# Performance work log

Measured on AMD Instinct MI355X. Metric: run time of the kernel, lower is better.

The kernel has to match this reference:

```python
import jax, jax.numpy as jnp
import numpy as np

N_ATOM_FEATS = 64
N_RBF = 10
N_CONV = 3
N_HIDDEN = 64
N_NODES = 50000
N_EDGES = 800000
N_GRAPHS = 512


def setup_inputs() -> dict:
    key = jax.random.key(0)
    ks = jax.random.split(key, 32)
    d = {}
    d["x_ids"] = jax.random.randint(ks[0], (N_NODES,), 0, 95)
    d["edge_index"] = jax.random.randint(ks[1], (2, N_EDGES), 0, N_NODES)
    d["edge_attr"] = jax.random.uniform(ks[2], (N_EDGES,), jnp.float32) * 6.0  # distances in [0,6)
    d["batch"] = jnp.sort(jax.random.randint(ks[3], (N_NODES,), 0, N_GRAPHS))
    # parameters
    def lin(k, fan_in, shape):
        return jax.random.normal(k, shape, jnp.float32) / np.sqrt(fan_in)
    d["emb"] = jax.random.normal(ks[4], (95, N_ATOM_FEATS), jnp.float32)
    d["blk_W1"] = lin(ks[5], N_ATOM_FEATS, (N_CONV, N_ATOM_FEATS, N_ATOM_FEATS))
    d["blk_b1"] = jnp.zeros((N_CONV, N_ATOM_FEATS), jnp.float32)
    d["blk_We"] = lin(ks[6], N_RBF, (N_CONV, N_RBF, N_ATOM_FEATS))
    d["blk_be"] = jnp.zeros((N_CONV, N_ATOM_FEATS), jnp.float32)
    d["blk_W2"] = lin(ks[7], N_ATOM_FEATS, (N_CONV, N_ATOM_FEATS, N_ATOM_FEATS))
    d["blk_b2"] = jnp.zeros((N_CONV, N_ATOM_FEATS), jnp.float32)
    d["Ws"] = lin(ks[8], N_ATOM_FEATS, (N_ATOM_FEATS, 2 * N_HIDDEN))
    d["bs"] = jnp.zeros((2 * N_HIDDEN,), jnp.float32)
    d["Wbg1"] = lin(ks[9], 2 * N_HIDDEN, (2 * N_HIDDEN, N_HIDDEN))
    d["bbg1"] = jnp.zeros((N_HIDDEN,), jnp.float32)
    d["Wbg2"] = lin(ks[10], N_HIDDEN, (N_HIDDEN, 1))
    d["bbg2"] = jnp.zeros((1,), jnp.float32)
    d["Weh1"] = lin(ks[11], 2 * N_HIDDEN, (2 * N_HIDDEN, N_HIDDEN))
    d["beh1"] = jnp.zeros((N_HIDDEN,), jnp.float32)
    d["Weh2"] = lin(ks[12], N_HIDDEN, (N_HIDDEN, 1))
    d["beh2"] = jnp.zeros((1,), jnp.float32)
    return d


def reference(x_ids, edge_index, edge_attr, batch, emb,
              blk_W1, blk_b1, blk_We, blk_be, blk_W2, blk_b2,
              Ws, bs, Wbg1, bbg1, Wbg2, bbg2, Weh1, beh1, Weh2, beh2):
    src, dst = edge_index[0], edge_index[1]
    # embedding lookup [N, F]
    x = emb[x_ids]
    # Gaussian smearing RBF: [E, n_rbf]
    offset = jnp.linspace(0.0, 6.0, N_RBF).astype(edge_attr.dtype)
    coeff = -0.5 / (offset[1] - offset[0]) ** 2
    e = jnp.exp(coeff * (edge_attr[:, None] - offset) ** 2)
    # interaction blocks (SchNet-style CFConv with residual)
    for i in range(N_CONV):
        h = x @ blk_W1[i] + blk_b1[i]                     # [N, F]
        f = e @ blk_We[i] + blk_be[i]                     # [E, F] edge filters
        m = h[src] * f                                    # [E, F] messages
        agg = jax.ops.segment_sum(m, dst, num_segments=N_NODES)
        x = x + agg @ blk_W2[i] + blk_b2[i]
        x = jax.nn.softplus(x)
    # global mean pool over graphs
    sums = jax.ops.segment_sum(x, batch, num_segments=N_GRAPHS)
    cnts = jax.ops.segment_sum(jnp.ones((x.shape[0],), x.dtype), batch, num_segments=N_GRAPHS)
    c = sums / jnp.maximum(cnts, 1.0)[:, None]
    c = jax.nn.relu(c @ Ws + bs)                          # [G, 2H]
    out_bg = jax.nn.relu(c @ Wbg1 + bbg1) @ Wbg2 + bbg2   # [G, 1]
    out_eh = jax.nn.relu(c @ Weh1 + beh1) @ Weh2 + beh2   # [G, 1]
    return (out_bg, out_eh)
```

## Files before the change

kernel.cpp:

```cpp
#include <hip/hip_runtime.h>
#include <hip/hip_fp16.h>
#include <cstddef>


#define BSH 8

#define RBF_C0 1.0f
#define RBF_C1 0.60653065971f
#define RBF_C2 0.13533528324f
#define RBF_C3 0.011108996538f
#define RBF_C4 3.3546262790e-4f
#define RBF_C5 3.7266531720e-6f
#define RBF_C6 1.5229979745e-8f
#define RBF_C7 2.2897348457e-11f
#define RBF_C8 1.2664165549e-14f
#define RBF_C9 2.5767043600e-18f

__device__ __forceinline__ float softplusf(float v) {
    return fmaxf(v, 0.0f) + log1pf(__expf(-fabsf(v)));
}

__device__ __forceinline__ float row_gemv(const float4* __restrict__ xr,
                                          const float w[64], float bj) {
    float a0 = bj, a1 = 0.f, a2 = 0.f, a3 = 0.f;
#pragma unroll
    for (int q = 0; q < 4; ++q) {
        float4 v0 = xr[4 * q + 0], v1 = xr[4 * q + 1];
        float4 v2 = xr[4 * q + 2], v3 = xr[4 * q + 3];
        a0 = fmaf(v0.x, w[16 * q + 0], a0);  a0 = fmaf(v0.y, w[16 * q + 1], a0);
        a0 = fmaf(v0.z, w[16 * q + 2], a0);  a0 = fmaf(v0.w, w[16 * q + 3], a0);
        a1 = fmaf(v1.x, w[16 * q + 4], a1);  a1 = fmaf(v1.y, w[16 * q + 5], a1);
        a1 = fmaf(v1.z, w[16 * q + 6], a1);  a1 = fmaf(v1.w, w[16 * q + 7], a1);
        a2 = fmaf(v2.x, w[16 * q + 8], a2);  a2 = fmaf(v2.y, w[16 * q + 9], a2);
        a2 = fmaf(v2.z, w[16 * q + 10], a2); a2 = fmaf(v2.w, w[16 * q + 11], a2);
        a3 = fmaf(v3.x, w[16 * q + 12], a3); a3 = fmaf(v3.y, w[16 * q + 13], a3);
        a3 = fmaf(v3.z, w[16 * q + 14], a3); a3 = fmaf(v3.w, w[16 * q + 15], a3);
    }
    return (a0 + a1) + (a2 + a3);
}

__device__ __forceinline__ float filt_ab(const float wp[10], float bj, float A, float B) {
    float P = wp[9];
    P = fmaf(B, P, wp[8]); P = fmaf(B, P, wp[7]); P = fmaf(B, P, wp[6]);
    P = fmaf(B, P, wp[5]); P = fmaf(B, P, wp[4]); P = fmaf(B, P, wp[3]);
    P = fmaf(B, P, wp[2]); P = fmaf(B, P, wp[1]); P = fmaf(B, P, wp[0]);
    return fmaf(A, P, bj);
}

__global__ void k_pre(const int* __restrict__ dst, int* __restrict__ deg,
                      const int* __restrict__ batch, int* __restrict__ gstart,
                      const int* __restrict__ ids, const float* __restrict__ emb,
                      const float* __restrict__ W1, const float* __restrict__ b1,
                      float* __restrict__ x, __half* __restrict__ hA,
                      int n_edges, int n_nodes, int n_graphs) {
    int tid = blockIdx.x * blockDim.x + threadIdx.x;
    int nth = gridDim.x * blockDim.x;
    for (int e = tid; e < n_edges; e += nth) atomicAdd(&deg[dst[e]], 1);
    for (int n = tid; n < n_nodes; n += nth) {
        int b = batch[n];
        int prev = (n == 0) ? -1 : batch[n - 1];
        for (int g = prev + 1; g <= b; ++g) gstart[g] = n;
        if (n == n_nodes - 1)
            for (int g = b + 1; g <= n_graphs; ++g) gstart[g] = n_nodes;
    }
    int lane = threadIdx.x & 63;
    int gw = __builtin_amdgcn_readfirstlane(tid >> 6);
    int nw = nth >> 6;
    float w[64];
#pragma unroll
    for (int k = 0; k < 64; ++k) w[k] = W1[k * 64 + lane];
    float bj = b1[lane];
    for (int n = gw; n < n_nodes; n += nw) {
        int id = __builtin_amdgcn_readfirstlane(ids[n]);
        const float4* xr = (const float4*)(emb + id * 64);
        float v = row_gemv(xr, w, bj);
        x[n * 64 + lane] = emb[id * 64 + lane];
        hA[n * 64 + lane] = __float2half(v);
    }
}

__global__ void k_scana(const int* __restrict__ deg, int* __restrict__ off_,
                        int* __restrict__ bsum, int n) {
    __shared__ int s[256];
    int i = blockIdx.x * 256 + threadIdx.x;
    int v = (i < n) ? deg[i] : 0;
    s[threadIdx.x] = v;
    __syncthreads();
    for (int off = 1; off < 256; off <<= 1) {
        int t = (threadIdx.x >= off) ? s[threadIdx.x - off] : 0;
        __syncthreads();
        s[threadIdx.x] += t;
        __syncthreads();
    }
    if (i < n) off_[i + 1] = s[threadIdx.x];
    if (threadIdx.x == 255) bsum[blockIdx.x] = s[255];
}

__global__ void k_scanb(int* __restrict__ bsum, int nb) {
    __shared__ int s[256];
    int v = ((int)threadIdx.x < nb) ? bsum[threadIdx.x] : 0;
    s[threadIdx.x] = v;
    __syncthreads();
    for (int off = 1; off < 256; off <<= 1) {
        int t = (threadIdx.x >= off) ? s[threadIdx.x - off] : 0;
        __syncthreads();
        s[threadIdx.x] += t;
        __syncthreads();
    }
    if ((int)threadIdx.x < nb) bsum[threadIdx.x] = s[threadIdx.x] - v;
}

__global__ void k_scanc(const int* __restrict__ deg, const int* __restrict__ bsum,
                        int* __restrict__ off_, int* __restrict__ cursor,
                        int* __restrict__ bcursor, int n) {
    int i = blockIdx.x * blockDim.x + threadIdx.x;
    if (i < n) {
        int incl = off_[i + 1] + bsum[i >> 8];
        off_[i + 1] = incl;
        cursor[i] = incl - deg[i];
        if (((i + 1) & ((1 << BSH) - 1)) == 0)
            bcursor[(i + 1) >> BSH] = incl;
    }
    if (i == 0) { off_[0] = 0; bcursor[0] = 0; }
}

__global__ __launch_bounds__(256) void k_scat1(
        const int* __restrict__ src, const int* __restrict__ dst,
        const float* __restrict__ dist, int* __restrict__ bcursor,
        int4* __restrict__ tmp, int n_edges) {
    __shared__ int hist[256], sofs[256], hbase[256], lcur[256];
    __shared__ int4 buf[1024];
    const int t = threadIdx.x;
    const int base = blockIdx.x << 10;

    hist[t] = 0;
    __syncthreads();

    int bk[4]; int4 pl[4];
#pragma unroll
    for (int i = 0; i < 4; ++i) {
        int e = base + (i << 8) + t;
        if (e < n_edges) {
            int d_ = dst[e];
            float dd = dist[e];
            float A = __expf(-1.125f * dd * dd);
            float B = __expf(1.5f * dd);
            pl[i] = make_int4(src[e] << 6, __float_as_int(A), __float_as_int(B), d_);
            bk[i] = d_ >> BSH;
            atomicAdd(&hist[bk[i]], 1);
        } else bk[i] = -1;
    }
    __syncthreads();

    int mycnt = hist[t];
    for (int off = 1; off < 256; off <<= 1) {
        int v = (t >= off) ? hist[t - off] : 0;
        __syncthreads();
        hist[t] += v;
        __syncthreads();
    }
    sofs[t] = hist[t] - mycnt;
    lcur[t] = hist[t] - mycnt;
    if (mycnt > 0) hbase[t] = atomicAdd(&bcursor[t], mycnt);
    __syncthreads();

#pragma unroll
    for (int i = 0; i < 4; ++i) {
        if (bk[i] >= 0) {
            int ls = atomicAdd(&lcur[bk[i]], 1);
            buf[ls] = pl[i];
        }
    }
    __syncthreads();

    int tot = n_edges - base; if (tot > 1024) tot = 1024;
    for (int s = t; s < tot; s += 256) {
        int4 p = buf[s];
        int b = p.w >> BSH;
        tmp[hbase[b] + (s - sofs[b])] = p;
    }
}

__global__ __launch_bounds__(256) void k_scat2(
        const int4* __restrict__ tmp, const int* __restrict__ off_,
        int* __restrict__ cursor, int4* __restrict__ psort, int n_nodes) {
    int b = blockIdx.x;
    int s0 = off_[b << BSH];
    int hi = (b + 1) << BSH; if (hi > n_nodes) hi = n_nodes;
    int s1 = off_[hi];
    int s = s0 + threadIdx.x;
    for (; s + 768 < s1; s += 1024) {
        int4 p0 = tmp[s], p1 = tmp[s + 256], p2 = tmp[s + 512], p3 = tmp[s + 768];
        int q0 = atomicAdd(&cursor[p0.w], 1);
        int q1 = atomicAdd(&cursor[p1.w], 1);
        int q2 = atomicAdd(&cursor[p2.w], 1);
        int q3 = atomicAdd(&cursor[p3.w], 1);
        psort[q0] = p0; psort[q1] = p1; psort[q2] = p2; psort[q3] = p3;
    }
    for (; s < s1; s += 256) {
        int4 p = tmp[s];
        psort[atomicAdd(&cursor[p.w], 1)] = p;
    }
}

__global__ void k_scatter(const int* __restrict__ src, const int* __restrict__ dst,
                          const float* __restrict__ dist, int* __restrict__ cursor,
                          int4* __restrict__ psort, int n_edges) {
    int e = blockIdx.x * blockDim.x + threadIdx.x;
    if (e >= n_edges) return;
    int t = dst[e];
    int pos = atomicAdd(&cursor[t], 1);
    float d = dist[e];
    float A = __expf(-1.125f * d * d);
    float B = __expf(1.5f * d);
    psort[pos] = make_int4(src[e] << 6, __float_as_int(A), __float_as_int(B), 0);
}

__global__ __launch_bounds__(256, 8) void k_gather(
        const int4* __restrict__ ps, const int* __restrict__ off,
        const __half* __restrict__ h,
        const float* __restrict__ We, const float* __restrict__ be,
        float* __restrict__ agg, int n_nodes) {
    int lane = threadIdx.x & 63;
    int gw = __builtin_amdgcn_readfirstlane((blockIdx.x * blockDim.x + threadIdx.x) >> 6);
    int nw = (gridDim.x * blockDim.x) >> 6;

    const float C[10] = {RBF_C0, RBF_C1, RBF_C2, RBF_C3, RBF_C4,
                         RBF_C5, RBF_C6, RBF_C7, RBF_C8, RBF_C9};
    float wp[10];
#pragma unroll
    for (int r = 0; r < 10; ++r) wp[r] = We[r * 64 + lane] * C[r];
    float bj = be[lane];

    for (int n = gw; n < n_nodes; n += nw) {
        int k0 = off[n], k1 = off[n + 1];
        float acc = 0.0f;
        int k = k0;
        for (; k + 8 <= k1; k += 8) {
            int4 p0 = ps[k + 0], p1 = ps[k + 1], p2 = ps[k + 2], p3 = ps[k + 3];
            int4 p4 = ps[k + 4], p5 = ps[k + 5], p6 = ps[k + 6], p7 = ps[k + 7];
            float g0 = __half2float(h[p0.x + lane]);
            float g1 = __half2float(h[p1.x + lane]);
            float g2 = __half2float(h[p2.x + lane]);
            float g3 = __half2float(h[p3.x + lane]);
            float g4 = __half2float(h[p4.x + lane]);
            float g5 = __half2float(h[p5.x + lane]);
            float g6 = __half2float(h[p6.x + lane]);
            float g7 = __half2float(h[p7.x + lane]);
            acc = fmaf(g0, filt_ab(wp, bj, __int_as_float(p0.y), __int_as_float(p0.z)), acc);
            acc = fmaf(g1, filt_ab(wp, bj, __int_as_float(p1.y), __int_as_float(p1.z)), acc);
            acc = fmaf(g2, filt_ab(wp, bj, __int_as_float(p2.y), __int_as_float(p2.z)), acc);
            acc = fmaf(g3, filt_ab(wp, bj, __int_as_float(p3.y), __int_as_float(p3.z)), acc);
            acc = fmaf(g4, filt_ab(wp, bj, __int_as_float(p4.y), __int_as_float(p4.z)), acc);
            acc = fmaf(g5, filt_ab(wp, bj, __int_as_float(p5.y), __int_as_float(p5.z)), acc);
            acc = fmaf(g6, filt_ab(wp, bj, __int_as_float(p6.y), __int_as_float(p6.z)), acc);
            acc = fmaf(g7, filt_ab(wp, bj, __int_as_float(p7.y), __int_as_float(p7.z)), acc);
        }
        for (; k + 4 <= k1; k += 4) {
            int4 p0 = ps[k + 0], p1 = ps[k + 1], p2 = ps[k + 2], p3 = ps[k + 3];
            float g0 = __half2float(h[p0.x + lane]);
            float g1 = __half2float(h[p1.x + lane]);
            float g2 = __half2float(h[p2.x + lane]);
            float g3 = __half2float(h[p3.x + lane]);
            acc = fmaf(g0, filt_ab(wp, bj, __int_as_float(p0.y), __int_as_float(p0.z)), acc);
            acc = fmaf(g1, filt_ab(wp, bj, __int_as_float(p1.y), __int_as_float(p1.z)), acc);
            acc = fmaf(g2, filt_ab(wp, bj, __int_as_float(p2.y), __int_as_float(p2.z)), acc);
            acc = fmaf(g3, filt_ab(wp, bj, __int_as_float(p3.y), __int_as_float(p3.z)), acc);
        }
        for (; k < k1; ++k) {
            int4 p = ps[k];
            float g = __half2float(h[p.x + lane]);
            acc = fmaf(g, filt_ab(wp, bj, __int_as_float(p.y), __int_as_float(p.z)), acc);
        }
        agg[n * 64 + lane] = acc;
    }
}

__global__ __launch_bounds__(512) void k_epi(
        const float* __restrict__ agg, float* __restrict__ x,
        const float* __restrict__ W2, const float* __restrict__ b2,
        const float* __restrict__ W1n, const float* __restrict__ b1n,
        __half* __restrict__ hout, int n_nodes, int do_next) {
    __shared__ float B1[64 * 65];
    const int t = threadIdx.x;
    const int lane = t & 63;
    const int wid = __builtin_amdgcn_readfirstlane(t >> 6);
    const int base = blockIdx.x << 6;
    const int nv = min(64, n_nodes - base);

#pragma unroll
    for (int i = 0; i < 2; ++i) {
        int f = ((wid * 2 + i) << 8) + (lane << 2);
        int r = f >> 6, c = f & 63;
        int rs = min(r, nv - 1);
        const float4 v = *(const float4*)(agg + (((size_t)(base + rs)) << 6) + c);
        B1[r * 65 + c + 0] = v.x; B1[r * 65 + c + 1] = v.y;
        B1[r * 65 + c + 2] = v.z; B1[r * 65 + c + 3] = v.w;
    }
    __syncthreads();

    float o[8];
#pragma unroll
    for (int jj = 0; jj < 8; ++jj) o[jj] = 0.0f;
#pragma unroll 4
    for (int k = 0; k < 64; ++k) {
        float a = B1[lane * 65 + k];
        const float4* w4 = (const float4*)(W2 + (k << 6) + (wid << 3));
        float4 wa = w4[0], wb = w4[1];
        o[0] = fmaf(a, wa.x, o[0]); o[1] = fmaf(a, wa.y, o[1]);
        o[2] = fmaf(a, wa.z, o[2]); o[3] = fmaf(a, wa.w, o[3]);
        o[4] = fmaf(a, wb.x, o[4]); o[5] = fmaf(a, wb.y, o[5]);
        o[6] = fmaf(a, wb.z, o[6]); o[7] = fmaf(a, wb.w, o[7]);
    }
    __syncthreads();

#pragma unroll
    for (int i = 0; i < 2; ++i) {
        int f = ((wid * 2 + i) << 8) + (lane << 2);
        int r = f >> 6, c = f & 63;
        int rs = min(r, nv - 1);
        const float4 v = *(const float4*)(x + (((size_t)(base + rs)) << 6) + c);
        B1[r * 65 + c + 0] = v.x; B1[r * 65 + c + 1] = v.y;
        B1[r * 65 + c + 2] = v.z; B1[r * 65 + c + 3] = v.w;
    }
    __syncthreads();

#pragma unroll
    for (int jj = 0; jj < 8; ++jj) {
        int j = (wid << 3) + jj;
        float xv = B1[lane * 65 + j];
        float xn = softplusf(xv + o[jj] + b2[j]);
        B1[lane * 65 + j] = xn;
    }
    __syncthreads();

#pragma unroll
    for (int rr = 0; rr < 8; ++rr) {
        int r = (wid << 3) + rr;
        if (r < nv) x[(((size_t)(base + r)) << 6) + lane] = B1[r * 65 + lane];
    }

    if (do_next) {
        float o2[8];
#pragma unroll
        for (int jj = 0; jj < 8; ++jj) o2[jj] = b1n[(wid << 3) + jj];
#pragma unroll 4
        for (int k = 0; k < 64; ++k) {
            float xk = B1[lane * 65 + k];
            const float4* w4 = (const float4*)(W1n + (k << 6) + (wid << 3));
            float4 wa = w4[0], wb = w4[1];
            o2[0] = fmaf(xk, wa.x, o2[0]); o2[1] = fmaf(xk, wa.y, o2[1]);
            o2[2] = fmaf(xk, wa.z, o2[2]); o2[3] = fmaf(xk, wa.w, o2[3]);
            o2[4] = fmaf(xk, wb.x, o2[4]); o2[5] = fmaf(xk, wb.y, o2[5]);
            o2[6] = fmaf(xk, wb.z, o2[6]); o2[7] = fmaf(xk, wb.w, o2[7]);
        }
        __syncthreads();
#pragma unroll
        for (int jj = 0; jj < 8; ++jj)
            B1[lane * 65 + (wid << 3) + jj] = o2[jj];
        __syncthreads();
#pragma unroll
        for (int rr = 0; rr < 8; ++rr) {
            int r = (wid << 3) + rr;
            if (r < nv)
                hout[(((size_t)(base + r)) << 6) + lane] = __float2half(B1[r * 65 + lane]);
        }
    }
}

__global__ __launch_bounds__(256, 6) void k_conv(
        const int4* __restrict__ ps, const int* __restrict__ off,
        const __half* __restrict__ h,
        const float* __restrict__ We, const float* __restrict__ be,
        const float* __restrict__ W2, const float* __restrict__ b2,
        const float* __restrict__ W1n, const float* __restrict__ b1n,
        float* __restrict__ x, __half* __restrict__ hout,
        int n_nodes, int do_next) {
    int lane = threadIdx.x & 63;
    int gw = __builtin_amdgcn_readfirstlane((blockIdx.x * blockDim.x + threadIdx.x) >> 6);
    int nw = (gridDim.x * blockDim.x) >> 6;

    const float C[10] = {RBF_C0, RBF_C1, RBF_C2, RBF_C3, RBF_C4,
                         RBF_C5, RBF_C6, RBF_C7, RBF_C8, RBF_C9};
    float wp[10];
#pragma unroll
    for (int r = 0; r < 10; ++r) wp[r] = We[r * 64 + lane] * C[r];
    float bj  = be[lane];
    float b2j = b2[lane];
    float b1j = do_next ? b1n[lane] : 0.0f;

    for (int n = gw; n < n_nodes; n += nw) {
        int k0 = off[n], k1 = off[n + 1];
        float acc = 0.0f;
        int k = k0;
        for (; k + 8 <= k1; k += 8) {
            int4 p0 = ps[k + 0], p1 = ps[k + 1], p2 = ps[k + 2], p3 = ps[k + 3];
            int4 p4 = ps[k + 4], p5 = ps[k + 5], p6 = ps[k + 6], p7 = ps[k + 7];
            float g0 = __half2float(h[p0.x + lane]);
            float g1 = __half2float(h[p1.x + lane]);
            float g2 = __half2float(h[p2.x + lane]);
            float g3 = __half2float(h[p3.x + lane]);
            float g4 = __half2float(h[p4.x + lane]);
            float g5 = __half2float(h[p5.x + lane]);
            float g6 = __half2float(h[p6.x + lane]);
            float g7 = __half2float(h[p7.x + lane]);
            acc = fmaf(g0, filt_ab(wp, bj, __int_as_float(p0.y), __int_as_float(p0.z)), acc);
            acc = fmaf(g1, filt_ab(wp, bj, __int_as_float(p1.y), __int_as_float(p1.z)), acc);
            acc = fmaf(g2, filt_ab(wp, bj, __int_as_float(p2.y), __int_as_float(p2.z)), acc);
            acc = fmaf(g3, filt_ab(wp, bj, __int_as_float(p3.y), __int_as_float(p3.z)), acc);
            acc = fmaf(g4, filt_ab(wp, bj, __int_as_float(p4.y), __int_as_float(p4.z)), acc);
            acc = fmaf(g5, filt_ab(wp, bj, __int_as_float(p5.y), __int_as_float(p5.z)), acc);
            acc = fmaf(g6, filt_ab(wp, bj, __int_as_float(p6.y), __int_as_float(p6.z)), acc);
            acc = fmaf(g7, filt_ab(wp, bj, __int_as_float(p7.y), __int_as_float(p7.z)), acc);
        }
        for (; k + 4 <= k1; k += 4) {
            int4 p0 = ps[k + 0], p1 = ps[k + 1], p2 = ps[k + 2], p3 = ps[k + 3];
            float g0 = __half2float(h[p0.x + lane]);
            float g1 = __half2float(h[p1.x + lane]);
            float g2 = __half2float(h[p2.x + lane]);
            float g3 = __half2float(h[p3.x + lane]);
            acc = fmaf(g0, filt_ab(wp, bj, __int_as_float(p0.y), __int_as_float(p0.z)), acc);
            acc = fmaf(g1, filt_ab(wp, bj, __int_as_float(p1.y), __int_as_float(p1.z)), acc);
            acc = fmaf(g2, filt_ab(wp, bj, __int_as_float(p2.y), __int_as_float(p2.z)), acc);
            acc = fmaf(g3, filt_ab(wp, bj, __int_as_float(p3.y), __int_as_float(p3.z)), acc);
        }
        for (; k < k1; ++k) {
            int4 p = ps[k];
            float g = __half2float(h[p.x + lane]);
            acc = fmaf(g, filt_ab(wp, bj, __int_as_float(p.y), __int_as_float(p.z)), acc);
        }
        float o0 = b2j + x[n * 64 + lane];
        float o1 = 0.f, o2 = 0.f, o3 = 0.f;
#pragma unroll 4
        for (int kk = 0; kk < 16; ++kk) {
            o0 = fmaf(__shfl(acc, kk),      W2[(kk)      * 64 + lane], o0);
            o1 = fmaf(__shfl(acc, kk + 16), W2[(kk + 16) * 64 + lane], o1);
            o2 = fmaf(__shfl(acc, kk + 32), W2[(kk + 32) * 64 + lane], o2);
            o3 = fmaf(__shfl(acc, kk + 48), W2[(kk + 48) * 64 + lane], o3);
        }
        float xn = softplusf((o0 + o1) + (o2 + o3));
        x[n * 64 + lane] = xn;
        if (do_next) {
            float q0 = b1j, q1 = 0.f, q2 = 0.f, q3 = 0.f;
#pragma unroll 4
            for (int kk = 0; kk < 16; ++kk) {
                q0 = fmaf(__shfl(xn, kk),      W1n[(kk)      * 64 + lane], q0);
                q1 = fmaf(__shfl(xn, kk + 16), W1n[(kk + 16) * 64 + lane], q1);
                q2 = fmaf(__shfl(xn, kk + 32), W1n[(kk + 32) * 64 + lane], q2);
                q3 = fmaf(__shfl(xn, kk + 48), W1n[(kk + 48) * 64 + lane], q3);
            }
            hout[n * 64 + lane] = __float2half((q0 + q1) + (q2 + q3));
        }
    }
}

__global__ void k_poolhead(const float* __restrict__ x, const int* __restrict__ gstart,
                           const float* __restrict__ Ws, const float* __restrict__ bs,
                           const float* __restrict__ Wbg1, const float* __restrict__ bbg1,
                           const float* __restrict__ Wbg2, const float* __restrict__ bbg2,
                           const float* __restrict__ Weh1, const float* __restrict__ beh1,
                           const float* __restrict__ Weh2, const float* __restrict__ beh2,
                           float* __restrict__ out, int n_graphs) {
    __shared__ float red[256];
    __shared__ float c[64];
    __shared__ float h1[128];
    int g = blockIdx.x;
    int t = threadIdx.x, j = t & 63, part = t >> 6;
    int s0 = gstart[g], s1 = gstart[g + 1];
    float acc = 0.0f;
    for (int n = s0 + part; n < s1; n += 4) acc += x[n * 64 + j];
    red[t] = acc;
    __syncthreads();
    if (part == 0)
        c[j] = (red[j] + red[64 + j] + red[128 + j] + red[192 + j]) /
               fmaxf((float)(s1 - s0), 1.0f);
    __syncthreads();
    if (t < 128) {
        float av = bs[t];
#pragma unroll 8
        for (int k = 0; k < 64; ++k) av = fmaf(c[k], Ws[k * 128 + t], av);
        h1[t] = fmaxf(av, 0.0f);
    }
    __syncthreads();
    if (t < 128) {
        const float* W1p = (t < 64) ? Wbg1 : Weh1;
        const float* b1p = (t < 64) ? bbg1 : beh1;
        const float* W2p = (t < 64) ? Wbg2 : Weh2;
        float b2v = (t < 64) ? bbg2[0] : beh2[0];
        int ln = t & 63;
        float a2 = b1p[ln];
#pragma unroll 8
        for (int k = 0; k < 128; ++k) a2 = fmaf(h1[k], W1p[k * 64 + ln], a2);
        a2 = fmaxf(a2, 0.0f);
        float pr = a2 * W2p[ln];
#pragma unroll
        for (int off = 32; off > 0; off >>= 1) pr += __shfl_down(pr, off);
        if (ln == 0) out[(t < 64 ? 0 : n_graphs) + g] = pr + b2v;
    }
}

extern "C" void kernel_launch(void* const* d_in, const int* in_sizes, int n_in,
                              void* d_out, int out_size, void* d_ws, size_t ws_size,
                              hipStream_t stream) {
    const int*   x_ids = (const int*)d_in[0];
    const int*   eidx  = (const int*)d_in[1];
    const float* eattr = (const float*)d_in[2];
    const int*   batch = (const int*)d_in[3];
    const float* emb   = (const float*)d_in[4];
    const float* W1    = (const float*)d_in[5];
    const float* b1    = (const float*)d_in[6];
    const float* We    = (const float*)d_in[7];
    const float* be    = (const float*)d_in[8];
    const float* W2    = (const float*)d_in[9];
    const float* b2    = (const float*)d_in[10];
    const float* Ws_   = (const float*)d_in[11];
    const float* bs_   = (const float*)d_in[12];
    const float* Wbg1  = (const float*)d_in[13];
    const float* bbg1  = (const float*)d_in[14];
    const float* Wbg2  = (const float*)d_in[15];
    const float* bbg2  = (const float*)d_in[16];
    const float* Weh1  = (const float*)d_in[17];
    const float* beh1  = (const float*)d_in[18];
    const float* Weh2  = (const float*)d_in[19];
    const float* beh2  = (const float*)d_in[20];

    int n_nodes  = in_sizes[0];
    int n_edges  = in_sizes[2];
    int n_graphs = out_size / 2;
    const int* src = eidx;
    const int* dst = eidx + n_edges;
    int nbuck = (n_nodes + (1 << BSH) - 1) >> BSH;
    int nbc = (nbuck < 256 ? 256 : nbuck) + 4;

    size_t base_bytes =
        (size_t)n_nodes * 64 * sizeof(float)
      + (size_t)n_nodes * 64 * sizeof(__half) * 2
      + (size_t)n_edges * sizeof(int4)
      + (size_t)n_nodes * sizeof(int) * 2
      + (size_t)(n_nodes + 1) * sizeof(int)
      + 256 * sizeof(int)
      + (size_t)(n_graphs + 1) * sizeof(int)
      + (size_t)nbc * sizeof(int);
    size_t agg_bytes = (size_t)n_nodes * 64 * sizeof(float);
    size_t tmp_bytes = (size_t)n_edges * sizeof(int4);
    size_t aggtmp_bytes = agg_bytes > tmp_bytes ? agg_bytes : tmp_bytes;
    int use_split = (ws_size >= base_bytes + aggtmp_bytes + 1024) ? 1 : 0;

    char* p = (char*)d_ws;
    float* x     = (float*)p;   p += (size_t)n_nodes * 64 * sizeof(float);
    __half* hA   = (__half*)p;  p += (size_t)n_nodes * 64 * sizeof(__half);
    __half* hB   = (__half*)p;  p += (size_t)n_nodes * 64 * sizeof(__half);
    int4* psort  = (int4*)p;    p += (size_t)n_edges * sizeof(int4);
    int* deg     = (int*)p;     p += (size_t)n_nodes * sizeof(int);
    int* off_    = (int*)p;     p += (size_t)(n_nodes + 1) * sizeof(int);
    int* cursor  = (int*)p;     p += (size_t)n_nodes * sizeof(int);
    int* bsum    = (int*)p;     p += 256 * sizeof(int);
    int* gstart  = (int*)p;     p += (size_t)(n_graphs + 1) * sizeof(int);
    int* bcursor = (int*)p;     p += (size_t)nbc * sizeof(int);
    float* agg   = (float*)p;
    int4* tmp    = (int4*)p;
    float* out   = (float*)d_out;

    int nchunks = (n_nodes + 255) / 256;
    int nbE = (n_edges + 255) / 256;
    int nbN = (n_nodes + 255) / 256;
    int ntile = (n_nodes + 63) / 64;
    int nbS1 = (n_edges + 1023) / 1024;

    hipMemsetAsync(deg, 0, (size_t)n_nodes * sizeof(int), stream);
    k_pre<<<nbE, 256, 0, stream>>>(dst, deg, batch, gstart, x_ids, emb, W1, b1,
                                   x, hA, n_edges, n_nodes, n_graphs);
    k_scana<<<nchunks, 256, 0, stream>>>(deg, off_, bsum, n_nodes);
    k_scanb<<<1, 256, 0, stream>>>(bsum, nchunks);
    k_scanc<<<nbN, 256, 0, stream>>>(deg, bsum, off_, cursor, bcursor, n_nodes);

    if (use_split) {
        k_scat1<<<nbS1, 256, 0, stream>>>(src, dst, eattr, bcursor, tmp, n_edges);
        k_scat2<<<nbuck, 256, 0, stream>>>(tmp, off_, cursor, psort, n_nodes);
        k_gather<<<4096, 256, 0, stream>>>(psort, off_, hA, We, be, agg, n_nodes);
        k_epi<<<ntile, 512, 0, stream>>>(agg, x, W2, b2,
                                         W1 + 4096, b1 + 64, hB, n_nodes, 1);
        k_gather<<<4096, 256, 0, stream>>>(psort, off_, hB, We + 640, be + 64, agg, n_nodes);
        k_epi<<<ntile, 512, 0, stream>>>(agg, x, W2 + 4096, b2 + 64,
                                         W1 + 8192, b1 + 128, hA, n_nodes, 1);
        k_gather<<<4096, 256, 0, stream>>>(psort, off_, hA, We + 1280, be + 128, agg, n_nodes);
        k_epi<<<ntile, 512, 0, stream>>>(agg, x, W2 + 8192, b2 + 128,
                                         nullptr, nullptr, nullptr, n_nodes, 0);
    } else {
        k_scatter<<<nbE, 256, 0, stream>>>(src, dst, eattr, cursor, psort, n_edges);
        k_conv<<<4096, 256, 0, stream>>>(psort, off_, hA, We, be, W2, b2,
                                         W1 + 4096, b1 + 64, x, hB, n_nodes, 1);
        k_conv<<<4096, 256, 0, stream>>>(psort, off_, hB, We + 640, be + 64,
                                         W2 + 4096, b2 + 64,
                                         W1 + 8192, b1 + 128, x, hA, n_nodes, 1);
        k_conv<<<4096, 256, 0, stream>>>(psort, off_, hA, We + 1280, be + 128,
                                         W2 + 8192, b2 + 128,
                                         nullptr, nullptr, x, nullptr, n_nodes, 0);
    }

    k_poolhead<<<n_graphs, 256, 0, stream>>>(x, gstart, Ws_, bs_, Wbg1, bbg1, Wbg2, bbg2,
                                             Weh1, beh1, Weh2, beh2, out, n_graphs);
}
```

Before: 380.9 us.

## Split gather into two feature-half passes with two edges per wavefront

The per-node gather kernel now handles only 32 of the 64 features per launch. Each half-wave processes alternate edges, and the two partial sums are combined with a cross-lane shuffle. Each layer launches the kernel twice, once per feature half, so the fp16 h footprint touched per pass is halved for better cache locality and each gathered row read is a 64-byte segment. The cost is that the edge list (psort) is read twice per layer, there are extra launches, and each h access is narrower.

```diff
diff --git a/kernel.cpp b/kernel.cpp
--- a/kernel.cpp
+++ b/kernel.cpp
@@ -216,12 +216,14 @@
     psort[pos] = make_int4(src[e] << 6, __float_as_int(A), __float_as_int(B), 0);
 }
 
-__global__ __launch_bounds__(256, 8) void k_gather(
+__global__ __launch_bounds__(256, 8) void k_gatherh(
         const int4* __restrict__ ps, const int* __restrict__ off,
         const __half* __restrict__ h,
         const float* __restrict__ We, const float* __restrict__ be,
-        float* __restrict__ agg, int n_nodes) {
+        float* __restrict__ agg, int n_nodes, int f0) {
     int lane = threadIdx.x & 63;
+    int half = lane >> 5;
+    int fl = (lane & 31) + f0;
     int gw = __builtin_amdgcn_readfirstlane((blockIdx.x * blockDim.x + threadIdx.x) >> 6);
     int nw = (gridDim.x * blockDim.x) >> 6;
 
@@ -229,24 +231,26 @@
                          RBF_C5, RBF_C6, RBF_C7, RBF_C8, RBF_C9};
     float wp[10];
 #pragma unroll
-    for (int r = 0; r < 10; ++r) wp[r] = We[r * 64 + lane] * C[r];
-    float bj = be[lane];
+    for (int r = 0; r < 10; ++r) wp[r] = We[r * 64 + fl] * C[r];
+    float bj = be[fl];
 
     for (int n = gw; n < n_nodes; n += nw) {
         int k0 = off[n], k1 = off[n + 1];
         float acc = 0.0f;
         int k = k0;
-        for (; k + 8 <= k1; k += 8) {
-            int4 p0 = ps[k + 0], p1 = ps[k + 1], p2 = ps[k + 2], p3 = ps[k + 3];
-            int4 p4 = ps[k + 4], p5 = ps[k + 5], p6 = ps[k + 6], p7 = ps[k + 7];
-            float g0 = __half2float(h[p0.x + lane]);
-            float g1 = __half2float(h[p1.x + lane]);
-            float g2 = __half2float(h[p2.x + lane]);
-            float g3 = __half2float(h[p3.x + lane]);
-            float g4 = __half2float(h[p4.x + lane]);
-            float g5 = __half2float(h[p5.x + lane]);
-            float g6 = __half2float(h[p6.x + lane]);
-            float g7 = __half2float(h[p7.x + lane]);
+        for (; k + 16 <= k1; k += 16) {
+            int4 p0 = ps[k + 0  + half], p1 = ps[k + 2  + half];
+            int4 p2 = ps[k + 4  + half], p3 = ps[k + 6  + half];
+            int4 p4 = ps[k + 8  + half], p5 = ps[k + 10 + half];
+            int4 p6 = ps[k + 12 + half], p7 = ps[k + 14 + half];
+            float g0 = __half2float(h[p0.x + fl]);
+            float g1 = __half2float(h[p1.x + fl]);
+            float g2 = __half2float(h[p2.x + fl]);
+            float g3 = __half2float(h[p3.x + fl]);
+            float g4 = __half2float(h[p4.x + fl]);
+            float g5 = __half2float(h[p5.x + fl]);
+            float g6 = __half2float(h[p6.x + fl]);
+            float g7 = __half2float(h[p7.x + fl]);
             acc = fmaf(g0, filt_ab(wp, bj, __int_as_float(p0.y), __int_as_float(p0.z)), acc);
             acc = fmaf(g1, filt_ab(wp, bj, __int_as_float(p1.y), __int_as_float(p1.z)), acc);
             acc = fmaf(g2, filt_ab(wp, bj, __int_as_float(p2.y), __int_as_float(p2.z)), acc);
@@ -256,23 +260,18 @@
             acc = fmaf(g6, filt_ab(wp, bj, __int_as_float(p6.y), __int_as_float(p6.z)), acc);
             acc = fmaf(g7, filt_ab(wp, bj, __int_as_float(p7.y), __int_as_float(p7.z)), acc);
         }
-        for (; k + 4 <= k1; k += 4) {
-            int4 p0 = ps[k + 0], p1 = ps[k + 1], p2 = ps[k + 2], p3 = ps[k + 3];
-            float g0 = __half2float(h[p0.x + lane]);
-            float g1 = __half2float(h[p1.x + lane]);
-            float g2 = __half2float(h[p2.x + lane]);
-            float g3 = __half2float(h[p3.x + lane]);
-            acc = fmaf(g0, filt_ab(wp, bj, __int_as_float(p0.y), __int_as_float(p0.z)), acc);
-            acc = fmaf(g1, filt_ab(wp, bj, __int_as_float(p1.y), __int_as_float(p1.z)), acc);
-            acc = fmaf(g2, filt_ab(wp, bj, __int_as_float(p2.y), __int_as_float(p2.z)), acc);
-            acc = fmaf(g3, filt_ab(wp, bj, __int_as_float(p3.y), __int_as_float(p3.z)), acc);
-        }
-        for (; k < k1; ++k) {
+        for (; k + 2 <= k1; k += 2) {
+            int4 p = ps[k + half];
+            float g = __half2float(h[p.x + fl]);
+            acc = fmaf(g, filt_ab(wp, bj, __int_as_float(p.y), __int_as_float(p.z)), acc);
+        }
+        if (k < k1 && half == 0) {
             int4 p = ps[k];
-            float g = __half2float(h[p.x + lane]);
+            float g = __half2float(h[p.x + fl]);
             acc = fmaf(g, filt_ab(wp, bj, __int_as_float(p.y), __int_as_float(p.z)), acc);
         }
-        agg[n * 64 + lane] = acc;
+        float tot = acc + __shfl_xor(acc, 32);
+        if (half == 0) agg[n * 64 + fl] = tot;
     }
 }
 
@@ -577,13 +576,16 @@
     if (use_split) {
         k_scat1<<<nbS1, 256, 0, stream>>>(src, dst, eattr, bcursor, tmp, n_edges);
         k_scat2<<<nbuck, 256, 0, stream>>>(tmp, off_, cursor, psort, n_nodes);
-        k_gather<<<4096, 256, 0, stream>>>(psort, off_, hA, We, be, agg, n_nodes);
+        k_gatherh<<<4096, 256, 0, stream>>>(psort, off_, hA, We, be, agg, n_nodes, 0);
+        k_gatherh<<<4096, 256, 0, stream>>>(psort, off_, hA, We, be, agg, n_nodes, 32);
         k_epi<<<ntile, 512, 0, stream>>>(agg, x, W2, b2,
                                          W1 + 4096, b1 + 64, hB, n_nodes, 1);
-        k_gather<<<4096, 256, 0, stream>>>(psort, off_, hB, We + 640, be + 64, agg, n_nodes);
+        k_gatherh<<<4096, 256, 0, stream>>>(psort, off_, hB, We + 640, be + 64, agg, n_nodes, 0);
+        k_gatherh<<<4096, 256, 0, stream>>>(psort, off_, hB, We + 640, be + 64, agg, n_nodes, 32);
         k_epi<<<ntile, 512, 0, stream>>>(agg, x, W2 + 4096, b2 + 64,
                                          W1 + 8192, b1 + 128, hA, n_nodes, 1);
-        k_gather<<<4096, 256, 0, stream>>>(psort, off_, hA, We + 1280, be + 128, agg, n_nodes);
+        k_gatherh<<<4096, 256, 0, stream>>>(psort, off_, hA, We + 1280, be + 128, agg, n_nodes, 0);
+        k_gatherh<<<4096, 256, 0, stream>>>(psort, off_, hA, We + 1280, be + 128, agg, n_nodes, 32);
         k_epi<<<ntile, 512, 0, stream>>>(agg, x, W2 + 8192, b2 + 128,
                                          nullptr, nullptr, nullptr, n_nodes, 0);
     } else {
```

Result: slower. 474.5 us (+24.6%).
